# Kernel tuning notes

Hardware: AMD Instinct MI355X
Metric: run time of the kernel (lower is better)

Reference implementation:

```python
import jax, jax.numpy as jnp
import numpy as np

INPUT_DIM = 1024
HIDDEN_DIM = 1024


def setup_inputs() -> dict:
    key = jax.random.key(0)
    k1, k2, k3, k4, k5 = jax.random.split(key, 5)
    B, T = 64, 512
    bound_h = 1.0 / np.sqrt(HIDDEN_DIM)
    bound_x = 1.0 / np.sqrt(INPUT_DIM)
    return {
        "x_seq": jax.random.normal(k1, (B, T, INPUT_DIM), dtype=jnp.float32),
        "W_h": jax.random.uniform(k2, (HIDDEN_DIM, HIDDEN_DIM), jnp.float32, -bound_h, bound_h),
        "b_h": jax.random.uniform(k3, (HIDDEN_DIM,), jnp.float32, -bound_h, bound_h),
        "W_x": jax.random.uniform(k4, (HIDDEN_DIM, INPUT_DIM), jnp.float32, -bound_x, bound_x),
        "b_x": jax.random.uniform(k5, (HIDDEN_DIM,), jnp.float32, -bound_x, bound_x),
    }


def reference(x_seq, W_h, b_h, W_x, b_x):
    # Precompute input projection for all timesteps as one batched GEMM:
    # xp: [B, T, H]
    xp = jnp.einsum("bti,hi->bth", x_seq, W_x) + b_x
    B = x_seq.shape[0]
    h0 = jnp.zeros((B, HIDDEN_DIM), dtype=x_seq.dtype)

    def step(h, xp_t):
        # h: [B, H], xp_t: [B, H]
        h_new = jnp.tanh(h @ W_h.T + b_h + xp_t)
        return h_new, None

    # scan over time: xp transposed to [T, B, H]
    h_final, _ = jax.lax.scan(step, h0, jnp.swapaxes(xp, 0, 1))
    return h_final  # [B, H] — last hidden state per batch element
```

## Files before the change

### kernel.cpp

```cpp
#include <hip/hip_runtime.h>
#include <cmath>


#define Bsz 64
#define Tsz 512
#define Hsz 1024

typedef float  f32x4 __attribute__((ext_vector_type(4)));
typedef short  s16x8 __attribute__((ext_vector_type(8)));

__device__ __forceinline__ unsigned short f2bf(float f) {
  unsigned u = __float_as_uint(f);
  u += 0x7fff + ((u >> 16) & 1);
  return (unsigned short)(u >> 16);
}

__device__ __forceinline__ void pack8(unsigned short* d, float4 v0, float4 v1) {
  d[0] = f2bf(v0.x); d[1] = f2bf(v0.y); d[2] = f2bf(v0.z); d[3] = f2bf(v0.w);
  d[4] = f2bf(v1.x); d[5] = f2bf(v1.y); d[6] = f2bf(v1.z); d[7] = f2bf(v1.w);
}

__device__ __forceinline__ float fast_tanh(float x) {
  float e = __expf(2.0f * x);
  return 1.0f - 2.0f / (e + 1.0f);
}

__global__ __launch_bounds__(256) void xp_gemm_kernel(
    const float* __restrict__ x, const float* __restrict__ Wx,
    const float* __restrict__ bx, const float* __restrict__ bh,
    float* __restrict__ xp) {
  __shared__ unsigned short Al[64 * 32];
  __shared__ unsigned short Bl[64 * 32];

  const int tid  = threadIdx.x;
  const int w    = tid >> 6;
  const int lane = tid & 63;
  const int m    = lane & 15;
  const int q    = lane >> 4;
  const int row0 = blockIdx.x * 64;
  const int col0 = blockIdx.y * 64;

  f32x4 acc[4];
#pragma unroll
  for (int i = 0; i < 4; ++i) acc[i] = (f32x4){0.f, 0.f, 0.f, 0.f};

  const int sr = tid >> 2;
  const int sc = tid & 3;
  const int sw = sc ^ ((sr >> 1) & 3);

  for (int kt = 0; kt < 32; ++kt) {
    const int k0 = kt * 32 + sc * 8;
    {
      const float* p = x + (size_t)(row0 + sr) * 1024 + k0;
      pack8(&Al[sr * 32 + sw * 8], *(const float4*)p, *(const float4*)(p + 4));
    }
    {
      const float* p = Wx + (size_t)(col0 + sr) * 1024 + k0;
      pack8(&Bl[sr * 32 + sw * 8], *(const float4*)p, *(const float4*)(p + 4));
    }
    __syncthreads();
    const int arow = w * 16 + m;
    s16x8 a = *(const s16x8*)&Al[arow * 32 + ((q ^ ((arow >> 1) & 3)) << 3)];
#pragma unroll
    for (int nt = 0; nt < 4; ++nt) {
      const int nrow = nt * 16 + m;
      s16x8 b = *(const s16x8*)&Bl[nrow * 32 + ((q ^ ((nrow >> 1) & 3)) << 3)];
      acc[nt] = __builtin_amdgcn_mfma_f32_16x16x32_bf16(a, b, acc[nt], 0, 0, 0);
    }
    __syncthreads();
  }

#pragma unroll
  for (int nt = 0; nt < 4; ++nt) {
    const int col  = col0 + nt * 16 + m;
    const float bias = bx[col] + bh[col];
#pragma unroll
    for (int r = 0; r < 4; ++r) {
      const int rowg = row0 + w * 16 + q * 4 + r;
      const int b = rowg >> 9;
      const int t = rowg & 511;
      xp[(size_t)t * (Bsz * Hsz) + b * Hsz + col] = acc[nt][r] + bias;
    }
  }
}

__global__ __launch_bounds__(128) void rnn_scan_kernel(
    const float* __restrict__ Wh, const float* __restrict__ xp,
    float* __restrict__ out,
    unsigned short* __restrict__ h0buf, unsigned short* __restrict__ h1buf,
    unsigned* __restrict__ flags) {
  __shared__ unsigned short Wl[32 * 1024];
  __shared__ unsigned short Tr[2][16 * 20];

  const int tid  = threadIdx.x;
  const int w    = tid >> 6;
  const int lane = tid & 63;
  const int m    = lane & 15;
  const int q    = lane >> 4;
  const int gb   = blockIdx.x >> 5;
  const int gj   = blockIdx.x & 31;
  const int rb   = gb * 16;
  const int j0   = gj * 32;

  for (int jr = 0; jr < 32; ++jr) {
    const float* p = Wh + (size_t)(j0 + jr) * 1024 + tid * 8;
    unsigned short* d = &Wl[jr * 1024 + ((((unsigned)tid) ^ (jr & 7)) << 3)];
    pack8(d, *(const float4*)p, *(const float4*)(p + 4));
  }
  __syncthreads();

  const int colg = j0 + w * 16 + m;
  const int jl   = w * 16 + m;

  unsigned* grpflags = flags + gb * 32 * 16;
  unsigned* myflag   = grpflags + gj * 16;
  const unsigned* pollflag = grpflags + (lane & 31) * 16;

  const int t_br = (lane >> 1) & 15;
  const int t_c0 = (lane >> 5) * 8 + (lane & 1) * 4;

  for (int t = 0; t < Tsz; ++t) {
    const unsigned short* hc = (t & 1) ? h1buf : h0buf;
    unsigned short*       hn = (t & 1) ? h0buf : h1buf;

    float xv[4];
#pragma unroll
    for (int r = 0; r < 4; ++r)
      xv[r] = xp[(size_t)t * (Bsz * Hsz) + (rb + q * 4 + r) * Hsz + colg];

    f32x4 acc0 = (f32x4){0.f, 0.f, 0.f, 0.f};
    f32x4 acc1 = (f32x4){0.f, 0.f, 0.f, 0.f};

    if (t > 0) {
      const unsigned long long* src =
          (const unsigned long long*)(hc + gb * 16384);
      const int loff = (q * 16 + m) * 2;

      unsigned v = __hip_atomic_load(pollflag, __ATOMIC_RELAXED,
                                     __HIP_MEMORY_SCOPE_AGENT);
      int wm = (int)__builtin_ctzll(~__ballot(v >= (unsigned)t) |
                                    0xFFFFFFFF00000000ull);
#pragma unroll
      for (int g = 0; g < 4; ++g) {
        while (wm < (g + 1) * 8) {
          __builtin_amdgcn_s_sleep(1);
          unsigned v2 = __hip_atomic_load(pollflag, __ATOMIC_RELAXED,
                                          __HIP_MEMORY_SCOPE_AGENT);
          wm = (int)__builtin_ctzll(~__ballot(v2 >= (unsigned)t) |
                                    0xFFFFFFFF00000000ull);
        }
        union { unsigned long long u[2]; s16x8 v; } a[8];
#pragma unroll
        for (int j = 0; j < 8; ++j) {
          const unsigned long long* cp = src + (g * 8 + j) * 128 + loff;
          a[j].u[0] = __hip_atomic_load(cp,     __ATOMIC_RELAXED, __HIP_MEMORY_SCOPE_AGENT);
          a[j].u[1] = __hip_atomic_load(cp + 1, __ATOMIC_RELAXED, __HIP_MEMORY_SCOPE_AGENT);
        }
#pragma unroll
        for (int j = 0; j < 8; ++j) {
          const int c = (g * 8 + j) * 4 + q;
          s16x8 b = *(const s16x8*)&Wl[jl * 1024 + ((c ^ (jl & 7)) << 3)];
          if (j & 1)
            acc1 = __builtin_amdgcn_mfma_f32_16x16x32_bf16(a[j].v, b, acc1, 0, 0, 0);
          else
            acc0 = __builtin_amdgcn_mfma_f32_16x16x32_bf16(a[j].v, b, acc0, 0, 0, 0);
        }
      }
    }
    f32x4 acc = acc0 + acc1;

    float hv[4];
#pragma unroll
    for (int r = 0; r < 4; ++r) hv[r] = fast_tanh(acc[r] + xv[r]);

    if (t == Tsz - 1) {
#pragma unroll
      for (int r = 0; r < 4; ++r)
        out[(rb + q * 4 + r) * Hsz + colg] = hv[r];
    } else {
      unsigned short* S = &Tr[w][0];
#pragma unroll
      for (int r = 0; r < 4; ++r)
        S[(q * 4 + r) * 20 + m] = f2bf(hv[r]);
      __asm__ __volatile__("" ::: "memory");
      unsigned long long tv =
          *(const volatile unsigned long long*)&S[t_br * 20 + t_c0];
      __asm__ __volatile__("" ::: "memory");
      unsigned long long* dst =
          (unsigned long long*)(hn + gb * 16384 + gj * 512 + w * 256) + lane;
      __hip_atomic_store(dst, tv, __ATOMIC_RELAXED, __HIP_MEMORY_SCOPE_AGENT);

      __syncthreads();
      if (tid == 0)
        __hip_atomic_store(myflag, (unsigned)(t + 1), __ATOMIC_RELAXED,
                           __HIP_MEMORY_SCOPE_AGENT);
    }
  }
}

extern "C" void kernel_launch(void* const* d_in, const int* in_sizes, int n_in,
                              void* d_out, int out_size, void* d_ws, size_t ws_size,
                              hipStream_t stream) {
  (void)in_sizes; (void)n_in; (void)out_size; (void)ws_size;
  const float* x  = (const float*)d_in[0];
  const float* Wh = (const float*)d_in[1];
  const float* bh = (const float*)d_in[2];
  const float* Wx = (const float*)d_in[3];
  const float* bx = (const float*)d_in[4];
  float* out = (float*)d_out;

  char* ws = (char*)d_ws;
  unsigned*       flags = (unsigned*)ws;
  unsigned short* h0    = (unsigned short*)(ws + 65536);
  unsigned short* h1    = (unsigned short*)(ws + 65536 + 131072);
  float*          xp    = (float*)(ws + (1 << 20));

  hipMemsetAsync(d_ws, 0, 16384, stream);

  dim3 g1(Bsz * Tsz / 64, Hsz / 64);
  xp_gemm_kernel<<<g1, dim3(256), 0, stream>>>(x, Wx, bx, bh, xp);
  rnn_scan_kernel<<<dim3(128), dim3(128), 0, stream>>>(Wh, xp, out, h0, h1, flags);
}
```

Baseline: 1.828 ms.

## Fuse input projection GEMM into recurrent scan and use per-wave flags

Removes the separate xp GEMM kernel. A light conversion kernel now casts x to bf16 in time-major layout, and each scan block multiplies its x_t slice by a shared-memory copy of Wx inside the time loop, before it waits on the recurrence dependency. This removes the fp32 xp write and read round trip and lets the input projection overlap with the wait for other blocks. The change also replaces the block-level __syncthreads plus single flag with a per-wave flag published after waitcnt, which makes the poll logic check flag pairs. In exchange, shared-memory use per block doubles and the x projection runs on only 128 blocks instead of a fully parallel GEMM, which could lengthen the serial critical path.

```diff
diff --git a/kernel.cpp b/kernel.cpp
--- a/kernel.cpp
+++ b/kernel.cpp
@@ -25,71 +25,25 @@
   return 1.0f - 2.0f / (e + 1.0f);
 }
 
-__global__ __launch_bounds__(256) void xp_gemm_kernel(
-    const float* __restrict__ x, const float* __restrict__ Wx,
-    const float* __restrict__ bx, const float* __restrict__ bh,
-    float* __restrict__ xp) {
-  __shared__ unsigned short Al[64 * 32];
-  __shared__ unsigned short Bl[64 * 32];
-
-  const int tid  = threadIdx.x;
-  const int w    = tid >> 6;
-  const int lane = tid & 63;
-  const int m    = lane & 15;
-  const int q    = lane >> 4;
-  const int row0 = blockIdx.x * 64;
-  const int col0 = blockIdx.y * 64;
-
-  f32x4 acc[4];
-#pragma unroll
-  for (int i = 0; i < 4; ++i) acc[i] = (f32x4){0.f, 0.f, 0.f, 0.f};
-
-  const int sr = tid >> 2;
-  const int sc = tid & 3;
-  const int sw = sc ^ ((sr >> 1) & 3);
-
-  for (int kt = 0; kt < 32; ++kt) {
-    const int k0 = kt * 32 + sc * 8;
-    {
-      const float* p = x + (size_t)(row0 + sr) * 1024 + k0;
-      pack8(&Al[sr * 32 + sw * 8], *(const float4*)p, *(const float4*)(p + 4));
-    }
-    {
-      const float* p = Wx + (size_t)(col0 + sr) * 1024 + k0;
-      pack8(&Bl[sr * 32 + sw * 8], *(const float4*)p, *(const float4*)(p + 4));
-    }
-    __syncthreads();
-    const int arow = w * 16 + m;
-    s16x8 a = *(const s16x8*)&Al[arow * 32 + ((q ^ ((arow >> 1) & 3)) << 3)];
-#pragma unroll
-    for (int nt = 0; nt < 4; ++nt) {
-      const int nrow = nt * 16 + m;
-      s16x8 b = *(const s16x8*)&Bl[nrow * 32 + ((q ^ ((nrow >> 1) & 3)) << 3)];
-      acc[nt] = __builtin_amdgcn_mfma_f32_16x16x32_bf16(a, b, acc[nt], 0, 0, 0);
-    }
-    __syncthreads();
-  }
-
-#pragma unroll
-  for (int nt = 0; nt < 4; ++nt) {
-    const int col  = col0 + nt * 16 + m;
-    const float bias = bx[col] + bh[col];
-#pragma unroll
-    for (int r = 0; r < 4; ++r) {
-      const int rowg = row0 + w * 16 + q * 4 + r;
-      const int b = rowg >> 9;
-      const int t = rowg & 511;
-      xp[(size_t)t * (Bsz * Hsz) + b * Hsz + col] = acc[nt][r] + bias;
-    }
-  }
+__global__ __launch_bounds__(128) void x_convert_kernel(
+    const float* __restrict__ x, unsigned short* __restrict__ xb) {
+  const int row = blockIdx.x;
+  const int b = row >> 9, t = row & 511;
+  const float* src = x + (size_t)row * Hsz + threadIdx.x * 8;
+  union { unsigned short s[8]; s16x8 v; } u;
+  pack8(u.s, *(const float4*)src, *(const float4*)(src + 4));
+  *(s16x8*)(xb + (size_t)t * (Bsz * Hsz) + b * Hsz + threadIdx.x * 8) = u.v;
 }
 
 __global__ __launch_bounds__(128) void rnn_scan_kernel(
-    const float* __restrict__ Wh, const float* __restrict__ xp,
+    const float* __restrict__ Wh, const float* __restrict__ Wx,
+    const float* __restrict__ bh, const float* __restrict__ bx,
+    const unsigned short* __restrict__ xb,
     float* __restrict__ out,
     unsigned short* __restrict__ h0buf, unsigned short* __restrict__ h1buf,
     unsigned* __restrict__ flags) {
   __shared__ unsigned short Wl[32 * 1024];
+  __shared__ unsigned short Wxl[32 * 1024];
   __shared__ unsigned short Tr[2][16 * 20];
 
   const int tid  = threadIdx.x;
@@ -103,18 +57,21 @@
   const int j0   = gj * 32;
 
   for (int jr = 0; jr < 32; ++jr) {
-    const float* p = Wh + (size_t)(j0 + jr) * 1024 + tid * 8;
-    unsigned short* d = &Wl[jr * 1024 + ((((unsigned)tid) ^ (jr & 7)) << 3)];
-    pack8(d, *(const float4*)p, *(const float4*)(p + 4));
+    const float* ph = Wh + (size_t)(j0 + jr) * 1024 + tid * 8;
+    const float* px = Wx + (size_t)(j0 + jr) * 1024 + tid * 8;
+    const int sw = ((((unsigned)tid) ^ (jr & 7)) << 3);
+    pack8(&Wl[jr * 1024 + sw],  *(const float4*)ph, *(const float4*)(ph + 4));
+    pack8(&Wxl[jr * 1024 + sw], *(const float4*)px, *(const float4*)(px + 4));
   }
   __syncthreads();
 
   const int colg = j0 + w * 16 + m;
   const int jl   = w * 16 + m;
+  const float bias = bx[colg] + bh[colg];
 
-  unsigned* grpflags = flags + gb * 32 * 16;
-  unsigned* myflag   = grpflags + gj * 16;
-  const unsigned* pollflag = grpflags + (lane & 31) * 16;
+  unsigned* grpflags = flags + gb * 64 * 16;
+  unsigned* myflag   = grpflags + (gj * 2 + w) * 16;
+  const unsigned* pollflag = grpflags + lane * 16;
 
   const int t_br = (lane >> 1) & 15;
   const int t_c0 = (lane >> 5) * 8 + (lane & 1) * 4;
@@ -123,13 +80,26 @@
     const unsigned short* hc = (t & 1) ? h1buf : h0buf;
     unsigned short*       hn = (t & 1) ? h0buf : h1buf;
 
-    float xv[4];
-#pragma unroll
-    for (int r = 0; r < 4; ++r)
-      xv[r] = xp[(size_t)t * (Bsz * Hsz) + (rb + q * 4 + r) * Hsz + colg];
-
     f32x4 acc0 = (f32x4){0.f, 0.f, 0.f, 0.f};
     f32x4 acc1 = (f32x4){0.f, 0.f, 0.f, 0.f};
+
+    const unsigned short* xrow = xb + (size_t)t * (Bsz * Hsz) + (rb + m) * Hsz;
+#pragma unroll
+    for (int g = 0; g < 4; ++g) {
+      s16x8 xa[8];
+#pragma unroll
+      for (int j = 0; j < 8; ++j)
+        xa[j] = *(const s16x8*)(xrow + (g * 8 + j) * 32 + q * 8);
+#pragma unroll
+      for (int j = 0; j < 8; ++j) {
+        const int c4 = (g * 8 + j) * 4 + q;
+        s16x8 b = *(const s16x8*)&Wxl[jl * 1024 + ((c4 ^ (jl & 7)) << 3)];
+        if (j & 1)
+          acc1 = __builtin_amdgcn_mfma_f32_16x16x32_bf16(xa[j], b, acc1, 0, 0, 0);
+        else
+          acc0 = __builtin_amdgcn_mfma_f32_16x16x32_bf16(xa[j], b, acc0, 0, 0, 0);
+      }
+    }
 
     if (t > 0) {
       const unsigned long long* src =
@@ -138,16 +108,18 @@
 
       unsigned v = __hip_atomic_load(pollflag, __ATOMIC_RELAXED,
                                      __HIP_MEMORY_SCOPE_AGENT);
-      int wm = (int)__builtin_ctzll(~__ballot(v >= (unsigned)t) |
-                                    0xFFFFFFFF00000000ull);
+      unsigned long long rdy = __ballot(v >= (unsigned)t);
+      unsigned long long nr = ~(rdy & (rdy >> 1)) & 0x5555555555555555ull;
+      int wm = nr ? (int)(__builtin_ctzll(nr) >> 1) : 32;
 #pragma unroll
       for (int g = 0; g < 4; ++g) {
         while (wm < (g + 1) * 8) {
           __builtin_amdgcn_s_sleep(1);
           unsigned v2 = __hip_atomic_load(pollflag, __ATOMIC_RELAXED,
                                           __HIP_MEMORY_SCOPE_AGENT);
-          wm = (int)__builtin_ctzll(~__ballot(v2 >= (unsigned)t) |
-                                    0xFFFFFFFF00000000ull);
+          unsigned long long r2 = __ballot(v2 >= (unsigned)t);
+          unsigned long long n2 = ~(r2 & (r2 >> 1)) & 0x5555555555555555ull;
+          wm = n2 ? (int)(__builtin_ctzll(n2) >> 1) : 32;
         }
         union { unsigned long long u[2]; s16x8 v; } a[8];
 #pragma unroll
@@ -158,8 +130,8 @@
         }
 #pragma unroll
         for (int j = 0; j < 8; ++j) {
-          const int c = (g * 8 + j) * 4 + q;
-          s16x8 b = *(const s16x8*)&Wl[jl * 1024 + ((c ^ (jl & 7)) << 3)];
+          const int c4 = (g * 8 + j) * 4 + q;
+          s16x8 b = *(const s16x8*)&Wl[jl * 1024 + ((c4 ^ (jl & 7)) << 3)];
           if (j & 1)
             acc1 = __builtin_amdgcn_mfma_f32_16x16x32_bf16(a[j].v, b, acc1, 0, 0, 0);
           else
@@ -171,7 +143,7 @@
 
     float hv[4];
 #pragma unroll
-    for (int r = 0; r < 4; ++r) hv[r] = fast_tanh(acc[r] + xv[r]);
+    for (int r = 0; r < 4; ++r) hv[r] = fast_tanh(acc[r] + bias);
 
     if (t == Tsz - 1) {
 #pragma unroll
@@ -190,10 +162,12 @@
           (unsigned long long*)(hn + gb * 16384 + gj * 512 + w * 256) + lane;
       __hip_atomic_store(dst, tv, __ATOMIC_RELAXED, __HIP_MEMORY_SCOPE_AGENT);
 
-      __syncthreads();
-      if (tid == 0)
+      __builtin_amdgcn_s_waitcnt(0);
+      __asm__ __volatile__("" ::: "memory");
+      if (lane == 0)
         __hip_atomic_store(myflag, (unsigned)(t + 1), __ATOMIC_RELAXED,
                            __HIP_MEMORY_SCOPE_AGENT);
+      __asm__ __volatile__("" ::: "memory");
     }
   }
 }
@@ -213,11 +187,11 @@
   unsigned*       flags = (unsigned*)ws;
   unsigned short* h0    = (unsigned short*)(ws + 65536);
   unsigned short* h1    = (unsigned short*)(ws + 65536 + 131072);
-  float*          xp    = (float*)(ws + (1 << 20));
+  unsigned short* xb    = (unsigned short*)(ws + (1 << 20));
 
   hipMemsetAsync(d_ws, 0, 16384, stream);
 
-  dim3 g1(Bsz * Tsz / 64, Hsz / 64);
-  xp_gemm_kernel<<<g1, dim3(256), 0, stream>>>(x, Wx, bx, bh, xp);
-  rnn_scan_kernel<<<dim3(128), dim3(128), 0, stream>>>(Wh, xp, out, h0, h1, flags);
+  x_convert_kernel<<<dim3(Bsz * Tsz), dim3(128), 0, stream>>>(x, xb);
+  rnn_scan_kernel<<<dim3(128), dim3(128), 0, stream>>>(
+      Wh, Wx, bh, bx, xb, out, h0, h1, flags);
 }
```

Measured after the change: 2.951 ms. +61.4%, slower.

## Fuse input-projection GEMM into the scan kernel with flag-based streaming

Applied to the files above, without the earlier changes.

Merges the input projection GEMM and the recurrent scan into one persistent kernel. 128 blocks run the scan while 256 extra blocks compute the xp tiles in time order and raise per-chunk counters, so the scan waits only on the chunk it needs. This overlaps the GEMM with the serial recurrence instead of running them back to back. The bias add moves into the scan. The design relies on all 384 blocks being co-resident and adds polling and atomic-store overhead.

```diff
diff --git a/kernel.cpp b/kernel.cpp
--- a/kernel.cpp
+++ b/kernel.cpp
@@ -25,175 +25,185 @@
   return 1.0f - 2.0f / (e + 1.0f);
 }
 
-__global__ __launch_bounds__(256) void xp_gemm_kernel(
-    const float* __restrict__ x, const float* __restrict__ Wx,
-    const float* __restrict__ bx, const float* __restrict__ bh,
-    float* __restrict__ xp) {
-  __shared__ unsigned short Al[64 * 32];
-  __shared__ unsigned short Bl[64 * 32];
+__global__ __launch_bounds__(128) void rnn_fused_kernel(
+    const float* __restrict__ Wh, const float* __restrict__ Wx,
+    const float* __restrict__ bh, const float* __restrict__ bx,
+    const float* __restrict__ x, float* __restrict__ xp,
+    float* __restrict__ out,
+    unsigned short* __restrict__ h0buf, unsigned short* __restrict__ h1buf,
+    unsigned* __restrict__ flags) {
+  __shared__ unsigned short Wl[32 * 1024];
+  __shared__ unsigned short Tr[2][16 * 20];
 
   const int tid  = threadIdx.x;
   const int w    = tid >> 6;
   const int lane = tid & 63;
   const int m    = lane & 15;
   const int q    = lane >> 4;
-  const int row0 = blockIdx.x * 64;
-  const int col0 = blockIdx.y * 64;
-
-  f32x4 acc[4];
-#pragma unroll
-  for (int i = 0; i < 4; ++i) acc[i] = (f32x4){0.f, 0.f, 0.f, 0.f};
-
-  const int sr = tid >> 2;
-  const int sc = tid & 3;
-  const int sw = sc ^ ((sr >> 1) & 3);
-
-  for (int kt = 0; kt < 32; ++kt) {
-    const int k0 = kt * 32 + sc * 8;
-    {
-      const float* p = x + (size_t)(row0 + sr) * 1024 + k0;
-      pack8(&Al[sr * 32 + sw * 8], *(const float4*)p, *(const float4*)(p + 4));
-    }
-    {
-      const float* p = Wx + (size_t)(col0 + sr) * 1024 + k0;
-      pack8(&Bl[sr * 32 + sw * 8], *(const float4*)p, *(const float4*)(p + 4));
+
+  if (blockIdx.x < 128) {
+    const int gb = blockIdx.x >> 5;
+    const int gj = blockIdx.x & 31;
+    const int rb = gb * 16;
+    const int j0 = gj * 32;
+
+    for (int jr = 0; jr < 32; ++jr) {
+      const float* p = Wh + (size_t)(j0 + jr) * 1024 + tid * 8;
+      unsigned short* d = &Wl[jr * 1024 + ((((unsigned)tid) ^ (jr & 7)) << 3)];
+      pack8(d, *(const float4*)p, *(const float4*)(p + 4));
     }
     __syncthreads();
+
+    const int colg = j0 + w * 16 + m;
+    const int jl   = w * 16 + m;
+    const float bias = bx[colg] + bh[colg];
+
+    unsigned* grpflags = flags + gb * 512;
+    unsigned* myflag   = grpflags + gj * 16;
+    const unsigned* pollflag = grpflags + (lane & 31) * 16;
+
+    const int t_br = (lane >> 1) & 15;
+    const int t_c0 = (lane >> 5) * 8 + (lane & 1) * 4;
+
+    for (int t = 0; t < Tsz; ++t) {
+      const unsigned short* hc = (t & 1) ? h1buf : h0buf;
+      unsigned short*       hn = (t & 1) ? h0buf : h1buf;
+
+      const unsigned* xcnt = flags + 2048 + ((t >> 3) << 4);
+      while (__hip_atomic_load(xcnt, __ATOMIC_RELAXED,
+                               __HIP_MEMORY_SCOPE_AGENT) < 256u)
+        __builtin_amdgcn_s_sleep(2);
+      __asm__ __volatile__("" ::: "memory");
+
+      float xv[4];
+#pragma unroll
+      for (int r = 0; r < 4; ++r)
+        xv[r] = xp[(size_t)(t * 64 + rb + q * 4 + r) * Hsz + colg];
+
+      f32x4 acc0 = (f32x4){0.f, 0.f, 0.f, 0.f};
+      f32x4 acc1 = (f32x4){0.f, 0.f, 0.f, 0.f};
+
+      if (t > 0) {
+        const unsigned long long* src =
+            (const unsigned long long*)(hc + gb * 16384);
+        const int loff = (q * 16 + m) * 2;
+
+        unsigned v = __hip_atomic_load(pollflag, __ATOMIC_RELAXED,
+                                       __HIP_MEMORY_SCOPE_AGENT);
+        int wm = (int)__builtin_ctzll(~__ballot(v >= (unsigned)t) |
+                                      0xFFFFFFFF00000000ull);
+#pragma unroll
+        for (int g = 0; g < 4; ++g) {
+          while (wm < (g + 1) * 8) {
+            __builtin_amdgcn_s_sleep(1);
+            unsigned v2 = __hip_atomic_load(pollflag, __ATOMIC_RELAXED,
+                                            __HIP_MEMORY_SCOPE_AGENT);
+            wm = (int)__builtin_ctzll(~__ballot(v2 >= (unsigned)t) |
+                                      0xFFFFFFFF00000000ull);
+          }
+          union { unsigned long long u[2]; s16x8 v; } a[8];
+#pragma unroll
+          for (int j = 0; j < 8; ++j) {
+            const unsigned long long* cp = src + (g * 8 + j) * 128 + loff;
+            a[j].u[0] = __hip_atomic_load(cp,     __ATOMIC_RELAXED, __HIP_MEMORY_SCOPE_AGENT);
+            a[j].u[1] = __hip_atomic_load(cp + 1, __ATOMIC_RELAXED, __HIP_MEMORY_SCOPE_AGENT);
+          }
+#pragma unroll
+          for (int j = 0; j < 8; ++j) {
+            const int c4 = (g * 8 + j) * 4 + q;
+            s16x8 b = *(const s16x8*)&Wl[jl * 1024 + ((c4 ^ (jl & 7)) << 3)];
+            if (j & 1)
+              acc1 = __builtin_amdgcn_mfma_f32_16x16x32_bf16(a[j].v, b, acc1, 0, 0, 0);
+            else
+              acc0 = __builtin_amdgcn_mfma_f32_16x16x32_bf16(a[j].v, b, acc0, 0, 0, 0);
+          }
+        }
+      }
+      f32x4 acc = acc0 + acc1;
+
+      float hv[4];
+#pragma unroll
+      for (int r = 0; r < 4; ++r) hv[r] = fast_tanh(acc[r] + xv[r] + bias);
+
+      if (t == Tsz - 1) {
+#pragma unroll
+        for (int r = 0; r < 4; ++r)
+          out[(rb + q * 4 + r) * Hsz + colg] = hv[r];
+      } else {
+        unsigned short* S = &Tr[w][0];
+#pragma unroll
+        for (int r = 0; r < 4; ++r)
+          S[(q * 4 + r) * 20 + m] = f2bf(hv[r]);
+        __asm__ __volatile__("" ::: "memory");
+        unsigned long long tv =
+            *(const volatile unsigned long long*)&S[t_br * 20 + t_c0];
+        __asm__ __volatile__("" ::: "memory");
+        unsigned long long* dst =
+            (unsigned long long*)(hn + gb * 16384 + gj * 512 + w * 256) + lane;
+        __hip_atomic_store(dst, tv, __ATOMIC_RELAXED, __HIP_MEMORY_SCOPE_AGENT);
+
+        __syncthreads();
+        if (tid == 0)
+          __hip_atomic_store(myflag, (unsigned)(t + 1), __ATOMIC_RELAXED,
+                             __HIP_MEMORY_SCOPE_AGENT);
+      }
+    }
+  } else {
+    unsigned short* Al = Wl;
+    unsigned short* Bl = Wl + 1024;
+
+    const int p = blockIdx.x - 128;
+    const int srA = tid >> 2, scA = tid & 3;
+    const int swA = scA ^ ((srA >> 1) & 3);
+    const int srB = tid >> 1, cB0 = (tid & 1) * 2, cB1 = cB0 + 1;
+    const int swB0 = cB0 ^ ((srB >> 1) & 3), swB1 = cB1 ^ ((srB >> 1) & 3);
     const int arow = w * 16 + m;
-    s16x8 a = *(const s16x8*)&Al[arow * 32 + ((q ^ ((arow >> 1) & 3)) << 3)];
-#pragma unroll
-    for (int nt = 0; nt < 4; ++nt) {
-      const int nrow = nt * 16 + m;
-      s16x8 b = *(const s16x8*)&Bl[nrow * 32 + ((q ^ ((nrow >> 1) & 3)) << 3)];
-      acc[nt] = __builtin_amdgcn_mfma_f32_16x16x32_bf16(a, b, acc[nt], 0, 0, 0);
-    }
-    __syncthreads();
-  }
-
-#pragma unroll
-  for (int nt = 0; nt < 4; ++nt) {
-    const int col  = col0 + nt * 16 + m;
-    const float bias = bx[col] + bh[col];
-#pragma unroll
-    for (int r = 0; r < 4; ++r) {
-      const int rowg = row0 + w * 16 + q * 4 + r;
-      const int b = rowg >> 9;
-      const int t = rowg & 511;
-      xp[(size_t)t * (Bsz * Hsz) + b * Hsz + col] = acc[nt][r] + bias;
-    }
-  }
-}
-
-__global__ __launch_bounds__(128) void rnn_scan_kernel(
-    const float* __restrict__ Wh, const float* __restrict__ xp,
-    float* __restrict__ out,
-    unsigned short* __restrict__ h0buf, unsigned short* __restrict__ h1buf,
-    unsigned* __restrict__ flags) {
-  __shared__ unsigned short Wl[32 * 1024];
-  __shared__ unsigned short Tr[2][16 * 20];
-
-  const int tid  = threadIdx.x;
-  const int w    = tid >> 6;
-  const int lane = tid & 63;
-  const int m    = lane & 15;
-  const int q    = lane >> 4;
-  const int gb   = blockIdx.x >> 5;
-  const int gj   = blockIdx.x & 31;
-  const int rb   = gb * 16;
-  const int j0   = gj * 32;
-
-  for (int jr = 0; jr < 32; ++jr) {
-    const float* p = Wh + (size_t)(j0 + jr) * 1024 + tid * 8;
-    unsigned short* d = &Wl[jr * 1024 + ((((unsigned)tid) ^ (jr & 7)) << 3)];
-    pack8(d, *(const float4*)p, *(const float4*)(p + 4));
-  }
-  __syncthreads();
-
-  const int colg = j0 + w * 16 + m;
-  const int jl   = w * 16 + m;
-
-  unsigned* grpflags = flags + gb * 32 * 16;
-  unsigned* myflag   = grpflags + gj * 16;
-  const unsigned* pollflag = grpflags + (lane & 31) * 16;
-
-  const int t_br = (lane >> 1) & 15;
-  const int t_c0 = (lane >> 5) * 8 + (lane & 1) * 4;
-
-  for (int t = 0; t < Tsz; ++t) {
-    const unsigned short* hc = (t & 1) ? h1buf : h0buf;
-    unsigned short*       hn = (t & 1) ? h0buf : h1buf;
-
-    float xv[4];
-#pragma unroll
-    for (int r = 0; r < 4; ++r)
-      xv[r] = xp[(size_t)t * (Bsz * Hsz) + (rb + q * 4 + r) * Hsz + colg];
-
-    f32x4 acc0 = (f32x4){0.f, 0.f, 0.f, 0.f};
-    f32x4 acc1 = (f32x4){0.f, 0.f, 0.f, 0.f};
-
-    if (t > 0) {
-      const unsigned long long* src =
-          (const unsigned long long*)(hc + gb * 16384);
-      const int loff = (q * 16 + m) * 2;
-
-      unsigned v = __hip_atomic_load(pollflag, __ATOMIC_RELAXED,
-                                     __HIP_MEMORY_SCOPE_AGENT);
-      int wm = (int)__builtin_ctzll(~__ballot(v >= (unsigned)t) |
-                                    0xFFFFFFFF00000000ull);
-#pragma unroll
-      for (int g = 0; g < 4; ++g) {
-        while (wm < (g + 1) * 8) {
-          __builtin_amdgcn_s_sleep(1);
-          unsigned v2 = __hip_atomic_load(pollflag, __ATOMIC_RELAXED,
-                                          __HIP_MEMORY_SCOPE_AGENT);
-          wm = (int)__builtin_ctzll(~__ballot(v2 >= (unsigned)t) |
-                                    0xFFFFFFFF00000000ull);
+    const int aoff = arow * 32 + ((q ^ ((arow >> 1) & 3)) << 3);
+
+    for (int i = 0; i < 64; ++i) {
+      const int tile = i * 256 + p;
+      const int mt = tile >> 4, ny = tile & 15;
+      const int r0 = mt * 32, n0 = ny * 64;
+      const int tt = r0 >> 6;
+      const int b0 = r0 & 63;
+
+      f32x4 acc[4];
+#pragma unroll
+      for (int k = 0; k < 4; ++k) acc[k] = (f32x4){0.f, 0.f, 0.f, 0.f};
+
+      for (int kt = 0; kt < 32; ++kt) {
+        const float* pa = x + ((size_t)(b0 + srA) * 512 + tt) * 1024 + kt * 32 + scA * 8;
+        pack8(&Al[srA * 32 + swA * 8], *(const float4*)pa, *(const float4*)(pa + 4));
+        const float* pb = Wx + (size_t)(n0 + srB) * 1024 + kt * 32 + cB0 * 8;
+        pack8(&Bl[srB * 32 + swB0 * 8], *(const float4*)pb, *(const float4*)(pb + 4));
+        pack8(&Bl[srB * 32 + swB1 * 8], *(const float4*)(pb + 8), *(const float4*)(pb + 12));
+        __syncthreads();
+        s16x8 a = *(const s16x8*)&Al[aoff];
+#pragma unroll
+        for (int nt = 0; nt < 4; ++nt) {
+          const int nrow = nt * 16 + m;
+          s16x8 b = *(const s16x8*)&Bl[nrow * 32 + ((q ^ ((nrow >> 1) & 3)) << 3)];
+          acc[nt] = __builtin_amdgcn_mfma_f32_16x16x32_bf16(a, b, acc[nt], 0, 0, 0);
         }
-        union { unsigned long long u[2]; s16x8 v; } a[8];
-#pragma unroll
-        for (int j = 0; j < 8; ++j) {
-          const unsigned long long* cp = src + (g * 8 + j) * 128 + loff;
-          a[j].u[0] = __hip_atomic_load(cp,     __ATOMIC_RELAXED, __HIP_MEMORY_SCOPE_AGENT);
-          a[j].u[1] = __hip_atomic_load(cp + 1, __ATOMIC_RELAXED, __HIP_MEMORY_SCOPE_AGENT);
+        __syncthreads();
+      }
+
+#pragma unroll
+      for (int nt = 0; nt < 4; ++nt) {
+        const int col = n0 + nt * 16 + m;
+#pragma unroll
+        for (int rr = 0; rr < 4; ++rr) {
+          const int r = r0 + w * 16 + q * 4 + rr;
+          __hip_atomic_store(xp + (size_t)r * 1024 + col, acc[nt][rr],
+                             __ATOMIC_RELAXED, __HIP_MEMORY_SCOPE_AGENT);
         }
-#pragma unroll
-        for (int j = 0; j < 8; ++j) {
-          const int c = (g * 8 + j) * 4 + q;
-          s16x8 b = *(const s16x8*)&Wl[jl * 1024 + ((c ^ (jl & 7)) << 3)];
-          if (j & 1)
-            acc1 = __builtin_amdgcn_mfma_f32_16x16x32_bf16(a[j].v, b, acc1, 0, 0, 0);
-          else
-            acc0 = __builtin_amdgcn_mfma_f32_16x16x32_bf16(a[j].v, b, acc0, 0, 0, 0);
-        }
-      }
-    }
-    f32x4 acc = acc0 + acc1;
-
-    float hv[4];
-#pragma unroll
-    for (int r = 0; r < 4; ++r) hv[r] = fast_tanh(acc[r] + xv[r]);
-
-    if (t == Tsz - 1) {
-#pragma unroll
-      for (int r = 0; r < 4; ++r)
-        out[(rb + q * 4 + r) * Hsz + colg] = hv[r];
-    } else {
-      unsigned short* S = &Tr[w][0];
-#pragma unroll
-      for (int r = 0; r < 4; ++r)
-        S[(q * 4 + r) * 20 + m] = f2bf(hv[r]);
+      }
+      __builtin_amdgcn_s_waitcnt(0);
       __asm__ __volatile__("" ::: "memory");
-      unsigned long long tv =
-          *(const volatile unsigned long long*)&S[t_br * 20 + t_c0];
-      __asm__ __volatile__("" ::: "memory");
-      unsigned long long* dst =
-          (unsigned long long*)(hn + gb * 16384 + gj * 512 + w * 256) + lane;
-      __hip_atomic_store(dst, tv, __ATOMIC_RELAXED, __HIP_MEMORY_SCOPE_AGENT);
-
       __syncthreads();
       if (tid == 0)
-        __hip_atomic_store(myflag, (unsigned)(t + 1), __ATOMIC_RELAXED,
-                           __HIP_MEMORY_SCOPE_AGENT);
+        __hip_atomic_fetch_add(flags + 2048 + (i << 4), 1u,
+                               __ATOMIC_RELAXED, __HIP_MEMORY_SCOPE_AGENT);
     }
   }
 }
@@ -217,7 +227,6 @@
 
   hipMemsetAsync(d_ws, 0, 16384, stream);
 
-  dim3 g1(Bsz * Tsz / 64, Hsz / 64);
-  xp_gemm_kernel<<<g1, dim3(256), 0, stream>>>(x, Wx, bx, bh, xp);
-  rnn_scan_kernel<<<dim3(128), dim3(128), 0, stream>>>(Wh, xp, out, h0, h1, flags);
-}
+  rnn_fused_kernel<<<dim3(384), dim3(128), 0, stream>>>(
+      Wh, Wx, bh, bx, x, xp, out, h0, h1, flags);
+}
```

Result: slower. 2.120 ms (+16.0%).
